# Kernel tuning notes

Measured on AMD Instinct MI355X. Metric: run time of the kernel, lower is better.

The kernel has to match this reference:

```python
import jax, jax.numpy as jnp
import numpy as np

NHEAD = 8
NEG_INF = -1e8

U, B, D = 2048, 4, 512
R, S, M = 64, 64, 64
Q = R + U + S
KV = M + R + U


def setup_inputs() -> dict:
    key = jax.random.key(0)
    ks = jax.random.split(key, 12)
    sd = 1.0 / np.sqrt(D)
    inp = {
        "utterance": jax.random.normal(ks[0], (U, B, D), jnp.float32),
        "lengths": jax.random.randint(ks[1], (B,), U // 2, U + 1),
        "right_context": jax.random.normal(ks[2], (R, B, D), jnp.float32),
        "summary": jax.random.normal(ks[3], (S, B, D), jnp.float32),
        "memory": jax.random.normal(ks[4], (M, B, D), jnp.float32),
        "attention_mask": jax.random.uniform(ks[5], (Q, KV)) < 0.3,
        "w_q": jax.random.normal(ks[6], (D, D), jnp.float32) * sd,
        "b_q": jax.random.normal(ks[7], (D,), jnp.float32) * 0.01,
        "w_kv": jax.random.normal(ks[8], (D, 2 * D), jnp.float32) * sd,
        "b_kv": jax.random.normal(ks[9], (2 * D,), jnp.float32) * 0.01,
        "w_out": jax.random.normal(ks[10], (D, D), jnp.float32) * sd,
        "b_out": jax.random.normal(ks[11], (D,), jnp.float32) * 0.01,
    }
    return inp


def reference(utterance, lengths, right_context, summary, memory,
              attention_mask, w_q, b_q, w_kv, b_kv, w_out, b_out):
    u_len, bsz, d = utterance.shape
    s_len = summary.shape[0]
    dh = d // NHEAD
    scaling = dh ** (-0.5)

    # Q = R + U + S ; KV = M + R + U
    q_in = jnp.concatenate([right_context, utterance, summary], axis=0)
    kv_in = jnp.concatenate([memory, right_context, utterance], axis=0)

    query = q_in @ w_q + b_q                      # (Q, B, D)
    kv = kv_in @ w_kv + b_kv                      # (KV, B, 2D)
    key_t, value = kv[..., :d], kv[..., d:]

    q_len, kv_len = query.shape[0], key_t.shape[0]
    q = query.reshape(q_len, bsz, NHEAD, dh)
    k = key_t.reshape(kv_len, bsz, NHEAD, dh)
    v = value.reshape(kv_len, bsz, NHEAD, dh)

    # (B, H, Q, KV) attention logits, computed in fp32 (matches .float())
    logits = jnp.einsum("qbhd,kbhd->bhqk", (q * scaling).astype(jnp.float32),
                        k.astype(jnp.float32))
    logits = jnp.where(attention_mask[None, None], NEG_INF, logits)

    if bsz > 1:
        # padding mask over keys: position j padded if j >= KV - U + lengths[b]
        pad = jnp.arange(kv_len)[None, :] >= (kv_len - u_len + lengths)[:, None]
        logits = jnp.where(pad[:, None, None, :], NEG_INF, logits)

    probs = jax.nn.softmax(logits, axis=-1).astype(q.dtype)
    attn = jnp.einsum("bhqk,kbhd->qbhd", probs, v).reshape(q_len, bsz, d)
    outputs = attn @ w_out + b_out                # (Q, B, D)

    out_rcu = outputs[: q_len - s_len]            # (R+U, B, D)
    out_mem = jnp.clip(outputs[q_len - s_len:], -10.0, 10.0)  # tanh_on_mem=False
    return out_rcu, out_mem[:-1]                  # memory output has length S-1
```

## Files before the change

### kernel.cpp

```cpp
#include <hip/hip_runtime.h>
#include <cmath>
#include <cstddef>

#define QLEN 2176
#define NROWS 8704
#define NEG_INF_V -100000000.0f
#define NMASK ((size_t)QLEN * (size_t)QLEN)
#define NBITW (4 * QLEN * 68)

typedef __attribute__((ext_vector_type(8))) short short8;
typedef __attribute__((ext_vector_type(4))) float f32x4;
typedef __attribute__((ext_vector_type(16))) float f32x16;
typedef unsigned short ushort_t;

#define MFMA16(A, B, C) __builtin_amdgcn_mfma_f32_16x16x32_bf16(A, B, C, 0, 0, 0)
#define MFMA32(A, B, C) __builtin_amdgcn_mfma_f32_32x32x16_bf16(A, B, C, 0, 0, 0)

#if __has_builtin(__builtin_amdgcn_exp2f)
#define EXP2(x) __builtin_amdgcn_exp2f(x)
#else
#define EXP2(x) __expf((x) * 0.6931471805599453f)
#endif

__device__ __forceinline__ ushort_t f2bf(float f) {
    unsigned int u = __builtin_bit_cast(unsigned int, f);
    u += 0x7FFFu + ((u >> 16) & 1u);
    return (ushort_t)(u >> 16);
}

__device__ __forceinline__ unsigned int cvtpk_bf16(float lo, float hi) {
    unsigned int r;
    asm volatile("v_cvt_pk_bf16_f32 %0, %1, %2" : "=v"(r) : "v"(lo), "v"(hi));
    return r;
}

__global__ __launch_bounds__(256) void detect_mask_kernel(
    const unsigned int* __restrict__ m, int* __restrict__ flag)
{
    __shared__ unsigned int r123, r01, r23;
    if (threadIdx.x == 0) { r123 = 0; r01 = 0; r23 = 0; }
    __syncthreads();
    unsigned int a123 = 0, a01 = 0, a23 = 0;
    #pragma unroll
    for (int i = 0; i < 16; ++i) {
        unsigned int w = m[threadIdx.x * 16 + i];
        a123 |= (w & 0xFFFFFF00u);
        a01  |= (w & 0x0000FFFFu);
        a23  |= (w & 0xFFFF0000u);
    }
    if (a123) atomicOr(&r123, 1u);
    if (a01)  atomicOr(&r01, 1u);
    if (a23)  atomicOr(&r23, 1u);
    __syncthreads();
    if (threadIdx.x == 0) {
        int f;
        if (!r123)            f = 0;
        else if (!r01 && r23) f = 2;
        else                  f = 1;
        *flag = f;
    }
}

__global__ __launch_bounds__(256) void canon_bits_kernel(
    const void* __restrict__ mraw, const int* __restrict__ flag,
    const int* __restrict__ lengths, unsigned int* __restrict__ bits)
{
    int idx = blockIdx.x * 256 + threadIdx.x;
    if (idx >= NBITW) return;
    int b = idx / (QLEN * 68);
    int rem = idx - b * (QLEN * 68);
    int q = rem / 68, w = rem - q * 68;
    int kv0 = w * 32;
    int f = *flag;
    unsigned int out = 0;
    if (f == 0) {
        const int* p = (const int*)mraw + (size_t)q * QLEN + kv0;
        #pragma unroll
        for (int j = 0; j < 32; ++j) out |= (p[j] != 0) ? (1u << j) : 0u;
    } else if (f == 2) {
        const float* p = (const float*)mraw + (size_t)q * QLEN + kv0;
        #pragma unroll
        for (int j = 0; j < 32; ++j) out |= (p[j] != 0.0f) ? (1u << j) : 0u;
    } else {
        const unsigned char* p = (const unsigned char*)mraw + (size_t)q * QLEN + kv0;
        #pragma unroll
        for (int j = 0; j < 32; ++j) out |= p[j] ? (1u << j) : 0u;
    }
    int n = (128 + lengths[b]) - kv0;
    unsigned int pm = (n <= 0) ? 0xFFFFFFFFu : (n >= 32 ? 0u : (0xFFFFFFFFu << n));
    bits[idx] = out | pm;
}

__global__ __launch_bounds__(256) void conv_concat(
    const float* __restrict__ s0, const float* __restrict__ s1, const float* __restrict__ s2,
    int b0, int b1, ushort_t* __restrict__ dst)
{
    int c = blockIdx.x * 256 + threadIdx.x;
    int row = c >> 6, ch = c & 63;
    if (row >= NROWS) return;
    const float* src;
    if (row < b0)      src = s0 + (size_t)row * 512;
    else if (row < b1) src = s1 + (size_t)(row - b0) * 512;
    else               src = s2 + (size_t)(row - b1) * 512;
    float4 v0 = *(const float4*)(src + ch * 8);
    float4 v1 = *(const float4*)(src + ch * 8 + 4);
    short8 o;
    o[0] = (short)f2bf(v0.x); o[1] = (short)f2bf(v0.y);
    o[2] = (short)f2bf(v0.z); o[3] = (short)f2bf(v0.w);
    o[4] = (short)f2bf(v1.x); o[5] = (short)f2bf(v1.y);
    o[6] = (short)f2bf(v1.z); o[7] = (short)f2bf(v1.w);
    *(short8*)(dst + (size_t)row * 512 + ch * 8) = o;
}

__global__ __launch_bounds__(256) void transpose_w(
    const float* __restrict__ W, ushort_t* __restrict__ Wt, int N)
{
    __shared__ float t[32][33];
    int n0 = blockIdx.x * 32, k0 = blockIdx.y * 32;
    int tx = threadIdx.x, ty = threadIdx.y;
    #pragma unroll
    for (int i = 0; i < 4; ++i)
        t[ty + 8 * i][tx] = W[(size_t)(k0 + ty + 8 * i) * N + n0 + tx];
    __syncthreads();
    #pragma unroll
    for (int i = 0; i < 4; ++i)
        Wt[(size_t)(n0 + ty + 8 * i) * 512 + k0 + tx] = f2bf(t[tx][ty + 8 * i]);
}

template<int MODE, int ASRC>
__global__ __launch_bounds__(256) void gemm_mfma(
    const ushort_t* __restrict__ A,
    const float* __restrict__ s0, const float* __restrict__ s1, const float* __restrict__ s2,
    int b0, int b1,
    const ushort_t* __restrict__ Bt,
    const float* __restrict__ bias, float scale,
    ushort_t* __restrict__ dst0, ushort_t* __restrict__ dst1,
    float* __restrict__ dstf)
{
    __shared__ __align__(16) ushort_t As[128][40];
    __shared__ __align__(16) ushort_t Bs[128][40];
    const int tid = threadIdx.x;
    const int wid = tid >> 6, lane = tid & 63, lr = lane & 15, lg = lane >> 4;
    const int wm = wid >> 1, wn = wid & 1;
    const int bm = blockIdx.x, bn = blockIdx.y;

    f32x4 acc[4][4] = {};

    for (int k0 = 0; k0 < 512; k0 += 32) {
        __syncthreads();
        #pragma unroll
        for (int p = 0; p < 2; ++p) {
            int c = p * 256 + tid;
            int row = c >> 2, ch = c & 3;
            if (ASRC == 0) {
                *(short8*)&As[row][ch * 8] =
                    *(const short8*)(A + (size_t)(bm * 128 + row) * 512 + k0 + ch * 8);
            } else {
                int gr = bm * 128 + row;
                const float* src;
                if (gr < b0)      src = s0 + (size_t)gr * 512;
                else if (gr < b1) src = s1 + (size_t)(gr - b0) * 512;
                else              src = s2 + (size_t)(gr - b1) * 512;
                float4 v0 = *(const float4*)(src + k0 + ch * 8);
                float4 v1 = *(const float4*)(src + k0 + ch * 8 + 4);
                short8 o;
                o[0] = (short)f2bf(v0.x); o[1] = (short)f2bf(v0.y);
                o[2] = (short)f2bf(v0.z); o[3] = (short)f2bf(v0.w);
                o[4] = (short)f2bf(v1.x); o[5] = (short)f2bf(v1.y);
                o[6] = (short)f2bf(v1.z); o[7] = (short)f2bf(v1.w);
                *(short8*)&As[row][ch * 8] = o;
            }
            *(short8*)&Bs[row][ch * 8] =
                *(const short8*)(Bt + (size_t)(bn * 128 + row) * 512 + k0 + ch * 8);
        }
        __syncthreads();
        short8 af[4], bf[4];
        #pragma unroll
        for (int i = 0; i < 4; ++i) {
            af[i] = *(const short8*)&As[wm * 64 + i * 16 + lr][lg * 8];
            bf[i] = *(const short8*)&Bs[wn * 64 + i * 16 + lr][lg * 8];
        }
        #pragma unroll
        for (int i = 0; i < 4; ++i)
            #pragma unroll
            for (int j = 0; j < 4; ++j)
                acc[i][j] = MFMA16(af[i], bf[j], acc[i][j]);
    }

    #pragma unroll
    for (int i = 0; i < 4; ++i) {
        #pragma unroll
        for (int j = 0; j < 4; ++j) {
            int gc = bn * 128 + wn * 64 + j * 16 + lr;
            float bv = bias[gc];
            #pragma unroll
            for (int r = 0; r < 4; ++r) {
                int gr = bm * 128 + wm * 64 + i * 16 + lg * 4 + r;
                float v = (acc[i][j][r] + bv) * scale;
                if (MODE == 0) {
                    int cc = gc;
                    ushort_t* d = dst0;
                    if (cc >= 512) { cc -= 512; d = dst1; }
                    int pos = gr >> 2, bb = gr & 3;
                    d[(((size_t)bb * 8 + (cc >> 6)) * QLEN + pos) * 64 + (cc & 63)] = f2bf(v);
                } else {
                    int q = gr >> 2, bb = gr & 3;
                    if (q < 2112) {
                        dstf[(size_t)gr * 512 + gc] = v;
                    } else if (q < 2175) {
                        float cv = fminf(10.0f, fmaxf(-10.0f, v));
                        dstf[(size_t)2112 * 4 * 512 + ((size_t)(q - 2112) * 4 + bb) * 512 + gc] = cv;
                    }
                }
            }
        }
    }
}

__global__ __launch_bounds__(256) void attn_mfma32(
    const ushort_t* __restrict__ Qa, const ushort_t* __restrict__ Ka,
    const ushort_t* __restrict__ Va,
    const unsigned int* __restrict__ mbits,
    ushort_t* __restrict__ attnb)
{
    __shared__ __align__(16) ushort_t Ks[64][72];
    __shared__ __align__(16) ushort_t Vt[64][72];

    const int swz = (blockIdx.x & 7) * 68 + (blockIdx.x >> 3);
    const int qt = swz % 17, bh = swz / 17;
    const int b = bh >> 3, h = bh & 7;
    const int tid = threadIdx.x;
    const int w = tid >> 6, lane = tid & 63;
    const int ql = lane & 31, hi = lane >> 5;
    const size_t hb = (size_t)bh * QLEN * 64;
    const int qrow = qt * 128 + w * 32 + ql;

    short8 bq[4];
    #pragma unroll
    for (int m = 0; m < 4; ++m)
        bq[m] = *(const short8*)(Qa + hb + (size_t)qrow * 64 + m * 16 + hi * 8);

    const unsigned int* mrow = mbits + ((size_t)b * QLEN + qrow) * 68;

    f32x16 oacc[2] = {};
    float lsum16[16];
    #pragma unroll
    for (int r = 0; r < 16; ++r) lsum16[r] = 0.0f;

    for (int kt = 0; kt < 34; ++kt) {
        const int k0 = kt * 64;
        __syncthreads();
        #pragma unroll
        for (int p2 = 0; p2 < 2; ++p2) {
            int c = p2 * 256 + tid;
            int row = c >> 3, ch = c & 7;
            *(short8*)&Ks[row][ch * 8] =
                *(const short8*)(Ka + hb + (size_t)(k0 + row) * 64 + ch * 8);
        }
        #pragma unroll
        for (int p2 = 0; p2 < 2; ++p2) {
            int c = p2 * 256 + tid;
            int kv = c & 63, ch = c >> 6;
            short8 v = *(const short8*)(Va + hb + (size_t)(k0 + kv) * 64 + ch * 8);
            #pragma unroll
            for (int i = 0; i < 8; ++i) Vt[ch * 8 + i][kv] = (ushort_t)v[i];
        }
        __syncthreads();

        f32x16 st[2] = {};
        __builtin_amdgcn_s_setprio(1);
        #pragma unroll
        for (int t = 0; t < 2; ++t)
            #pragma unroll
            for (int m = 0; m < 4; ++m) {
                short8 ak = *(const short8*)&Ks[t * 32 + ql][m * 16 + hi * 8];
                st[t] = MFMA32(ak, bq[m], st[t]);
            }
        __builtin_amdgcn_s_setprio(0);

        unsigned int wm0 = mrow[kt * 2]     >> (hi * 4);
        unsigned int wm1 = mrow[kt * 2 + 1] >> (hi * 4);
        float p[2][16];
        #pragma unroll
        for (int t = 0; t < 2; ++t) {
            unsigned int wt = t ? wm1 : wm0;
            #pragma unroll
            for (int r = 0; r < 16; ++r) {
                const int rl = (r & 3) + 8 * (r >> 2);
                float x = ((wt >> rl) & 1u) ? NEG_INF_V : st[t][r];
                p[t][r] = EXP2(x);
            }
        }
        #pragma unroll
        for (int r = 0; r < 16; ++r) lsum16[r] += p[0][r] + p[1][r];

        unsigned int bw[4][4];
        #pragma unroll
        for (int c = 0; c < 4; ++c) {
            const int t0 = c >> 1, s0 = (2 * c) & 3, s1 = s0 + 1;
            unsigned int A = cvtpk_bf16(p[t0][4 * s0 + 0], p[t0][4 * s0 + 1]);
            unsigned int B = cvtpk_bf16(p[t0][4 * s1 + 0], p[t0][4 * s1 + 1]);
            unsigned int C = cvtpk_bf16(p[t0][4 * s0 + 2], p[t0][4 * s0 + 3]);
            unsigned int D = cvtpk_bf16(p[t0][4 * s1 + 2], p[t0][4 * s1 + 3]);
            asm volatile("v_permlane32_swap_b32 %0, %1" : "+v"(A), "+v"(B));
            asm volatile("v_permlane32_swap_b32 %0, %1" : "+v"(C), "+v"(D));
            bw[c][0] = A; bw[c][1] = C; bw[c][2] = B; bw[c][3] = D;
        }

        __builtin_amdgcn_s_setprio(1);
        #pragma unroll
        for (int c = 0; c < 4; ++c) {
            uint4 t4; t4.x = bw[c][0]; t4.y = bw[c][1]; t4.z = bw[c][2]; t4.w = bw[c][3];
            short8 bp = __builtin_bit_cast(short8, t4);
            #pragma unroll
            for (int dt = 0; dt < 2; ++dt) {
                short8 av = *(const short8*)&Vt[dt * 32 + ql][c * 16 + hi * 8];
                oacc[dt] = MFMA32(av, bp, oacc[dt]);
            }
        }
        __builtin_amdgcn_s_setprio(0);
    }

    #pragma unroll
    for (int s = 8; s; s >>= 1)
        #pragma unroll
        for (int r = 0; r < s; ++r) lsum16[r] += lsum16[r + s];
    float lsum = lsum16[0] + __shfl_xor(lsum16[0], 32);

    float inv = 1.0f / lsum;
    #pragma unroll
    for (int dt = 0; dt < 2; ++dt)
        #pragma unroll
        for (int s = 0; s < 4; ++s) {
            unsigned int lo = (unsigned int)f2bf(oacc[dt][4 * s + 0] * inv)
                            | ((unsigned int)f2bf(oacc[dt][4 * s + 1] * inv) << 16);
            unsigned int hi2 = (unsigned int)f2bf(oacc[dt][4 * s + 2] * inv)
                             | ((unsigned int)f2bf(oacc[dt][4 * s + 3] * inv) << 16);
            uint2 pk; pk.x = lo; pk.y = hi2;
            *(uint2*)(attnb + ((size_t)qrow * 4 + b) * 512 + h * 64 + dt * 32 + 8 * s + 4 * hi) = pk;
        }
}

extern "C" void kernel_launch(void* const* d_in, const int* in_sizes, int n_in,
                              void* d_out, int out_size, void* d_ws, size_t ws_size,
                              hipStream_t stream) {
    const float* utterance     = (const float*)d_in[0];
    const int*   lengths       = (const int*)d_in[1];
    const float* right_context = (const float*)d_in[2];
    const float* summary       = (const float*)d_in[3];
    const float* memory        = (const float*)d_in[4];
    const void*  mask_raw      = d_in[5];
    const float* w_q   = (const float*)d_in[6];
    const float* b_q   = (const float*)d_in[7];
    const float* w_kv  = (const float*)d_in[8];
    const float* b_kv  = (const float*)d_in[9];
    const float* w_out = (const float*)d_in[10];
    const float* b_out = (const float*)d_in[11];
    float* out = (float*)d_out;

    char* ws = (char*)d_ws;
    const size_t SZ = (size_t)NROWS * 512 * 2;
    ushort_t* kvin   = (ushort_t*)(ws);
    ushort_t* q_attn = (ushort_t*)(ws + SZ);
    ushort_t* k_attn = (ushort_t*)(ws + 2 * SZ);
    ushort_t* v_attn = (ushort_t*)(ws + 3 * SZ);
    ushort_t* attnb  = (ushort_t*)(ws + 4 * SZ);
    ushort_t* wtq    = (ushort_t*)(ws + 5 * SZ);
    ushort_t* wtkv   = wtq + (size_t)512 * 512;
    ushort_t* wtout  = wtkv + (size_t)1024 * 512;
    unsigned int* mbits = (unsigned int*)(wtout + (size_t)512 * 512);
    int* maskflag = (int*)(mbits + NBITW);

    detect_mask_kernel<<<1, 256, 0, stream>>>((const unsigned int*)mask_raw, maskflag);
    canon_bits_kernel<<<(NBITW + 255) / 256, 256, 0, stream>>>(mask_raw, maskflag, lengths, mbits);

    conv_concat<<<2176, 256, 0, stream>>>(memory, right_context, utterance, 256, 512, kvin);

    transpose_w<<<dim3(16, 16), dim3(32, 8), 0, stream>>>(w_q, wtq, 512);
    transpose_w<<<dim3(32, 16), dim3(32, 8), 0, stream>>>(w_kv, wtkv, 1024);
    transpose_w<<<dim3(16, 16), dim3(32, 8), 0, stream>>>(w_out, wtout, 512);

    const float qscale = 0.125f * 1.4426950408889634f;
    gemm_mfma<0, 1><<<dim3(68, 4), 256, 0, stream>>>(
        nullptr, right_context, utterance, summary, 256, 8448,
        wtq, b_q, qscale, q_attn, q_attn, nullptr);
    gemm_mfma<0, 0><<<dim3(68, 8), 256, 0, stream>>>(
        kvin, nullptr, nullptr, nullptr, 0, 0,
        wtkv, b_kv, 1.0f, k_attn, v_attn, nullptr);

    attn_mfma32<<<544, 256, 0, stream>>>(q_attn, k_attn, v_attn, mbits, attnb);

    gemm_mfma<1, 0><<<dim3(68, 4), 256, 0, stream>>>(
        attnb, nullptr, nullptr, nullptr, 0, 0,
        wtout, b_out, 1.0f, nullptr, nullptr, out);
}
```

Before: 182.9 us.

## Vectorize mask canonicalization, fuse weight transposes, pre-transpose V, use direct LDS loads

The mask bit-packing kernel now reads rows with 16-byte vector loads instead of scalar loops. The three weight-transpose launches are merged into one. The GEMM tiles now load through global_load_lds with an XOR-swizzled LDS layout in place of padded rows. V is transposed once in a separate kernel, so the attention kernel can copy Vt tiles with vector stores instead of scattering them element by element. This adds one launch and extra workspace, and it depends on the swizzle matching the lane-to-LDS-address mapping of global_load_lds.

Measured after the change: 202.6 us. 10.7% more time.

```diff
diff --git a/kernel.cpp b/kernel.cpp
--- a/kernel.cpp
+++ b/kernel.cpp
@@ -32,6 +32,12 @@
     unsigned int r;
     asm volatile("v_cvt_pk_bf16_f32 %0, %1, %2" : "=v"(r) : "v"(lo), "v"(hi));
     return r;
+}
+
+__device__ __forceinline__ void gload16(const void* g, void* l) {
+    __builtin_amdgcn_global_load_lds(
+        (const __attribute__((address_space(1))) void*)g,
+        (__attribute__((address_space(3))) void*)l, 16, 0, 0);
 }
 
 __global__ __launch_bounds__(256) void detect_mask_kernel(
@@ -73,18 +79,27 @@
     int kv0 = w * 32;
     int f = *flag;
     unsigned int out = 0;
-    if (f == 0) {
-        const int* p = (const int*)mraw + (size_t)q * QLEN + kv0;
-        #pragma unroll
-        for (int j = 0; j < 32; ++j) out |= (p[j] != 0) ? (1u << j) : 0u;
-    } else if (f == 2) {
-        const float* p = (const float*)mraw + (size_t)q * QLEN + kv0;
-        #pragma unroll
-        for (int j = 0; j < 32; ++j) out |= (p[j] != 0.0f) ? (1u << j) : 0u;
+    if (f == 1) {
+        const uint4* p = (const uint4*)((const unsigned char*)mraw + (size_t)q * QLEN + kv0);
+        uint4 va = p[0], vb = p[1];
+        unsigned int ws2[8] = {va.x, va.y, va.z, va.w, vb.x, vb.y, vb.z, vb.w};
+        #pragma unroll
+        for (int ww = 0; ww < 8; ++ww) {
+            unsigned int x = ws2[ww];
+            #pragma unroll
+            for (int j = 0; j < 4; ++j)
+                out |= ((x >> (8 * j)) & 0xFFu) ? (1u << (ww * 4 + j)) : 0u;
+        }
     } else {
-        const unsigned char* p = (const unsigned char*)mraw + (size_t)q * QLEN + kv0;
-        #pragma unroll
-        for (int j = 0; j < 32; ++j) out |= p[j] ? (1u << j) : 0u;
+        const uint4* p = (const uint4*)((const unsigned int*)mraw + (size_t)q * QLEN + kv0);
+        #pragma unroll
+        for (int g2 = 0; g2 < 8; ++g2) {
+            uint4 v = p[g2];
+            out |= (v.x ? 1u : 0u) << (g2 * 4);
+            out |= (v.y ? 2u : 0u) << (g2 * 4);
+            out |= (v.z ? 4u : 0u) << (g2 * 4);
+            out |= (v.w ? 8u : 0u) << (g2 * 4);
+        }
     }
     int n = (128 + lengths[b]) - kv0;
     unsigned int pm = (n <= 0) ? 0xFFFFFFFFu : (n >= 32 ? 0u : (0xFFFFFFFFu << n));
@@ -112,12 +127,19 @@
     *(short8*)(dst + (size_t)row * 512 + ch * 8) = o;
 }
 
-__global__ __launch_bounds__(256) void transpose_w(
-    const float* __restrict__ W, ushort_t* __restrict__ Wt, int N)
+__global__ __launch_bounds__(256) void transpose_w_all(
+    const float* __restrict__ w_q, const float* __restrict__ w_kv,
+    const float* __restrict__ w_out,
+    ushort_t* __restrict__ wtq, ushort_t* __restrict__ wtkv, ushort_t* __restrict__ wtout)
 {
     __shared__ float t[32][33];
-    int n0 = blockIdx.x * 32, k0 = blockIdx.y * 32;
-    int tx = threadIdx.x, ty = threadIdx.y;
+    int bx = blockIdx.x;
+    const float* W; ushort_t* Wt; int N, nb;
+    if (bx < 16)      { W = w_q;   Wt = wtq;   N = 512;  nb = bx; }
+    else if (bx < 48) { W = w_kv;  Wt = wtkv;  N = 1024; nb = bx - 16; }
+    else              { W = w_out; Wt = wtout; N = 512;  nb = bx - 48; }
+    int n0 = nb * 32, k0 = blockIdx.y * 32;
+    int tx = threadIdx.x & 31, ty = threadIdx.x >> 5;
     #pragma unroll
     for (int i = 0; i < 4; ++i)
         t[ty + 8 * i][tx] = W[(size_t)(k0 + ty + 8 * i) * N + n0 + tx];
@@ -125,6 +147,32 @@
     #pragma unroll
     for (int i = 0; i < 4; ++i)
         Wt[(size_t)(n0 + ty + 8 * i) * 512 + k0 + tx] = f2bf(t[tx][ty + 8 * i]);
+}
+
+__global__ __launch_bounds__(256) void transpose_v(
+    const ushort_t* __restrict__ va, ushort_t* __restrict__ vt)
+{
+    __shared__ ushort_t t[64][72];
+    const int q0 = blockIdx.x * 64;
+    const size_t hb = (size_t)blockIdx.y * QLEN * 64;
+    const size_t hbt = (size_t)blockIdx.y * 64 * QLEN;
+    const int tid = threadIdx.x;
+    #pragma unroll
+    for (int p = 0; p < 2; ++p) {
+        int c = p * 256 + tid;
+        int r = c >> 3, col = (c & 7) * 8;
+        *(short8*)&t[r][col] = *(const short8*)(va + hb + (size_t)(q0 + r) * 64 + col);
+    }
+    __syncthreads();
+    #pragma unroll
+    for (int p = 0; p < 2; ++p) {
+        int c = p * 256 + tid;
+        int d = c >> 3, qo = (c & 7) * 8;
+        short8 o;
+        #pragma unroll
+        for (int j = 0; j < 8; ++j) o[j] = (short)t[qo + j][d];
+        *(short8*)(vt + hbt + (size_t)d * QLEN + q0 + qo) = o;
+    }
 }
 
 template<int MODE, int ASRC>
@@ -137,8 +185,8 @@
     ushort_t* __restrict__ dst0, ushort_t* __restrict__ dst1,
     float* __restrict__ dstf)
 {
-    __shared__ __align__(16) ushort_t As[128][40];
-    __shared__ __align__(16) ushort_t Bs[128][40];
+    __shared__ __align__(16) ushort_t As[128][32];
+    __shared__ __align__(16) ushort_t Bs[128][32];
     const int tid = threadIdx.x;
     const int wid = tid >> 6, lane = tid & 63, lr = lane & 15, lg = lane >> 4;
     const int wm = wid >> 1, wn = wid & 1;
@@ -149,36 +197,39 @@
     for (int k0 = 0; k0 < 512; k0 += 32) {
         __syncthreads();
         #pragma unroll
-        for (int p = 0; p < 2; ++p) {
-            int c = p * 256 + tid;
-            int row = c >> 2, ch = c & 3;
+        for (int i = 0; i < 2; ++i) {
+            const int q = wid * 128 + 64 * i + lane;
+            const int row = q >> 2, pc = q & 3;
+            const int sc = pc ^ (row & 3);
             if (ASRC == 0) {
-                *(short8*)&As[row][ch * 8] =
-                    *(const short8*)(A + (size_t)(bm * 128 + row) * 512 + k0 + ch * 8);
+                gload16(A + (size_t)(bm * 128 + row) * 512 + k0 + sc * 8,
+                        (ushort_t*)As + (size_t)(wid * 128 + 64 * i) * 8);
             } else {
                 int gr = bm * 128 + row;
                 const float* src;
                 if (gr < b0)      src = s0 + (size_t)gr * 512;
                 else if (gr < b1) src = s1 + (size_t)(gr - b0) * 512;
                 else              src = s2 + (size_t)(gr - b1) * 512;
-                float4 v0 = *(const float4*)(src + k0 + ch * 8);
-                float4 v1 = *(const float4*)(src + k0 + ch * 8 + 4);
+                float4 v0 = *(const float4*)(src + k0 + sc * 8);
+                float4 v1 = *(const float4*)(src + k0 + sc * 8 + 4);
                 short8 o;
                 o[0] = (short)f2bf(v0.x); o[1] = (short)f2bf(v0.y);
                 o[2] = (short)f2bf(v0.z); o[3] = (short)f2bf(v0.w);
                 o[4] = (short)f2bf(v1.x); o[5] = (short)f2bf(v1.y);
                 o[6] = (short)f2bf(v1.z); o[7] = (short)f2bf(v1.w);
-                *(short8*)&As[row][ch * 8] = o;
+                *(short8*)&As[row][pc * 8] = o;
             }
-            *(short8*)&Bs[row][ch * 8] =
-                *(const short8*)(Bt + (size_t)(bn * 128 + row) * 512 + k0 + ch * 8);
+            gload16(Bt + (size_t)(bn * 128 + row) * 512 + k0 + sc * 8,
+                    (ushort_t*)Bs + (size_t)(wid * 128 + 64 * i) * 8);
         }
         __syncthreads();
         short8 af[4], bf[4];
         #pragma unroll
         for (int i = 0; i < 4; ++i) {
-            af[i] = *(const short8*)&As[wm * 64 + i * 16 + lr][lg * 8];
-            bf[i] = *(const short8*)&Bs[wn * 64 + i * 16 + lr][lg * 8];
+            const int ra = wm * 64 + i * 16 + lr;
+            const int rb = wn * 64 + i * 16 + lr;
+            af[i] = *(const short8*)&As[ra][(lg ^ (ra & 3)) * 8];
+            bf[i] = *(const short8*)&Bs[rb][(lg ^ (rb & 3)) * 8];
         }
         #pragma unroll
         for (int i = 0; i < 4; ++i)
@@ -219,7 +270,7 @@
 
 __global__ __launch_bounds__(256) void attn_mfma32(
     const ushort_t* __restrict__ Qa, const ushort_t* __restrict__ Ka,
-    const ushort_t* __restrict__ Va,
+    const ushort_t* __restrict__ Vtg,
     const unsigned int* __restrict__ mbits,
     ushort_t* __restrict__ attnb)
 {
@@ -233,6 +284,7 @@
     const int w = tid >> 6, lane = tid & 63;
     const int ql = lane & 31, hi = lane >> 5;
     const size_t hb = (size_t)bh * QLEN * 64;
+    const size_t hbv = (size_t)bh * 64 * QLEN;
     const int qrow = qt * 128 + w * 32 + ql;
 
     short8 bq[4];
@@ -253,17 +305,16 @@
         #pragma unroll
         for (int p2 = 0; p2 < 2; ++p2) {
             int c = p2 * 256 + tid;
-            int row = c >> 3, ch = c & 7;
-            *(short8*)&Ks[row][ch * 8] =
-                *(const short8*)(Ka + hb + (size_t)(k0 + row) * 64 + ch * 8);
+            int row = c >> 3, ch = (c & 7) * 8;
+            *(short8*)&Ks[row][ch] =
+                *(const short8*)(Ka + hb + (size_t)(k0 + row) * 64 + ch);
         }
         #pragma unroll
         for (int p2 = 0; p2 < 2; ++p2) {
             int c = p2 * 256 + tid;
-            int kv = c & 63, ch = c >> 6;
-            short8 v = *(const short8*)(Va + hb + (size_t)(k0 + kv) * 64 + ch * 8);
-            #pragma unroll
-            for (int i = 0; i < 8; ++i) Vt[ch * 8 + i][kv] = (ushort_t)v[i];
+            int d = c >> 3, kc = (c & 7) * 8;
+            *(short8*)&Vt[d][kc] =
+                *(const short8*)(Vtg + hbv + (size_t)d * QLEN + k0 + kc);
         }
         __syncthreads();
 
@@ -365,7 +416,8 @@
     ushort_t* k_attn = (ushort_t*)(ws + 2 * SZ);
     ushort_t* v_attn = (ushort_t*)(ws + 3 * SZ);
     ushort_t* attnb  = (ushort_t*)(ws + 4 * SZ);
-    ushort_t* wtq    = (ushort_t*)(ws + 5 * SZ);
+    ushort_t* vtg    = (ushort_t*)(ws + 5 * SZ);
+    ushort_t* wtq    = (ushort_t*)(ws + 6 * SZ);
     ushort_t* wtkv   = wtq + (size_t)512 * 512;
     ushort_t* wtout  = wtkv + (size_t)1024 * 512;
     unsigned int* mbits = (unsigned int*)(wtout + (size_t)512 * 512);
@@ -376,9 +428,7 @@
 
     conv_concat<<<2176, 256, 0, stream>>>(memory, right_context, utterance, 256, 512, kvin);
 
-    transpose_w<<<dim3(16, 16), dim3(32, 8), 0, stream>>>(w_q, wtq, 512);
-    transpose_w<<<dim3(32, 16), dim3(32, 8), 0, stream>>>(w_kv, wtkv, 1024);
-    transpose_w<<<dim3(16, 16), dim3(32, 8), 0, stream>>>(w_out, wtout, 512);
+    transpose_w_all<<<dim3(64, 16), 256, 0, stream>>>(w_q, w_kv, w_out, wtq, wtkv, wtout);
 
     const float qscale = 0.125f * 1.4426950408889634f;
     gemm_mfma<0, 1><<<dim3(68, 4), 256, 0, stream>>>(
@@ -388,7 +438,8 @@
         kvin, nullptr, nullptr, nullptr, 0, 0,
         wtkv, b_kv, 1.0f, k_attn, v_attn, nullptr);
 
-    attn_mfma32<<<544, 256, 0, stream>>>(q_attn, k_attn, v_attn, mbits, attnb);
+    transpose_v<<<dim3(34, 32), 256, 0, stream>>>(v_attn, vtg);
+    attn_mfma32<<<544, 256, 0, stream>>>(q_attn, k_attn, vtg, mbits, attnb);
 
     gemm_mfma<1, 0><<<dim3(68, 4), 256, 0, stream>>>(
         attnb, nullptr, nullptr, nullptr, 0, 0,
```
